# Kernel tuning notes

Hardware: AMD Instinct MI355X
Metric: run time of the kernel (lower is better)

Reference implementation:

```python
import jax, jax.numpy as jnp
import numpy as np

N, D, E, K, L, NF, VOCAB = 100000, 128, 600000, 3, 3, 9, 100
BN_EPS = 1e-5
S = 0.05


def setup_inputs() -> dict:
    key = jax.random.key(0)
    ks = jax.random.split(key, 8)
    return {
        "x": jax.random.randint(ks[0], (N, NF), 0, VOCAB),
        "k_edges": jax.random.randint(ks[1], (K, 2, E), 0, N),
        "emb_tables": jax.random.normal(ks[2], (NF, VOCAB, D), jnp.float32) * S,
        "W1": jax.random.normal(ks[3], (L, D, 2 * D), jnp.float32) * S,
        "b1": jnp.zeros((L, 2 * D), jnp.float32),
        "g1": jnp.ones((L, 2 * D), jnp.float32),
        "be1": jnp.zeros((L, 2 * D), jnp.float32),
        "W2": jax.random.normal(ks[4], (L, 2 * D, D), jnp.float32) * S,
        "b2": jnp.zeros((L, D), jnp.float32),
        "eps": jnp.zeros((L,), jnp.float32),
        "alpha": jnp.zeros((L, K), jnp.float32),
        "bn_g": jnp.ones((L, D), jnp.float32),
        "bn_b": jnp.zeros((L, D), jnp.float32),
    }


def _bn(h, g, b):
    # training-mode BatchNorm1d over the node (batch) axis
    mu = h.mean(axis=0)
    var = h.var(axis=0)
    return (h - mu) * jax.lax.rsqrt(var + BN_EPS) * g + b


def _gin(h, src, dst, eps_l, W1_l, b1_l, g1_l, be1_l, W2_l, b2_l):
    # NodeGINConv (train_eps): mlp((1+eps)*x + sum_{j->i} x_j)
    agg = jax.ops.segment_sum(h[src], dst, num_segments=N)  # [N, D]
    z = (1.0 + eps_l) * h + agg
    z = jax.nn.relu(_bn(z @ W1_l + b1_l, g1_l, be1_l))  # [N, 2D]
    return z @ W2_l + b2_l  # [N, D]


def reference(x, k_edges, emb_tables, W1, b1, g1, be1, W2, b2, eps, alpha, bn_g, bn_b):
    # AtomEncoder: sum of per-feature embedding lookups -> [N, D]
    h = jnp.take_along_axis(
        emb_tables.transpose(1, 0, 2),  # [VOCAB, NF, D]
        x.T[..., None].transpose(1, 0, 2) * 0 + 0,  # placeholder avoided below
        axis=0,
    ) if False else emb_tables[jnp.arange(NF)[None, :], x].sum(axis=1)
    for l in range(L):
        # one shared wrapped GIN conv applied to each of the K relational edge sets
        msgs = jax.vmap(
            lambda e: _gin(h, e[0], e[1], eps[l], W1[l], b1[l], g1[l], be1[l], W2[l], b2[l])
        )(k_edges)  # [K, N, D]
        a = jax.nn.softmax(alpha[l])  # [K]
        h = jnp.einsum('knd,k->nd', msgs, a)
        h = jax.nn.relu(_bn(h, bn_g[l], bn_b[l]))  # dropout p=0 / eval -> identity
    return h
```

## Files before the change

### kernel.cpp

```cpp
#include <hip/hip_runtime.h>

#define NV     100000
#define DD     128
#define D2     256
#define EE     600000
#define KK     3
#define LL     3
#define NFEAT  9
#define VOCABS 100

#define NBKT   196
#define BCAP   8192

typedef __attribute__((ext_vector_type(8))) short short8;
typedef __attribute__((ext_vector_type(4))) float f32x4;
typedef __attribute__((ext_vector_type(2))) float f32x2;
typedef __attribute__((ext_vector_type(4))) unsigned int uint4v;

#define PA      0
#define PA2     8
#define PB2     136
#define PA1K(k) (264 + (k)*512)
#define PB1K(k) (264 + (k)*512 + 256)

#define ZS(k)  ((k)*512)
#define ZQ(k)  ((k)*512 + 256)
#define HSUM   1536
#define HSQ    1664

#define HB_OFF   ((size_t)0)
#define ZIN_OFF  ((size_t)25700000)
#define HNB_OFF  ((size_t)102500000)
#define O_BASE   ((size_t)128100000)

__device__ __forceinline__ unsigned short f2bf(float f) {
    union { float f; unsigned int u; } v; v.f = f;
    return (unsigned short)((v.u + 0x7FFFu + ((v.u >> 16) & 1u)) >> 16);
}
__device__ __forceinline__ float bf2f(unsigned short u) {
    union { unsigned int u; float f; } v; v.u = ((unsigned int)u) << 16;
    return v.f;
}
__device__ __forceinline__ f32x2 up2(unsigned int v) {
    union { unsigned int u[2]; f32x2 f; } w;
    w.u[0] = v << 16;
    w.u[1] = v & 0xFFFF0000u;
    return w.f;
}

__global__ void k_embed(const int* __restrict__ x, const float* __restrict__ emb,
                        unsigned short* __restrict__ hb) {
    int id = blockIdx.x*256 + threadIdx.x;
    int n = id >> 5, q = id & 31;
    if (n >= NV) {
        if (n < NV + 8) *(unsigned long long*)(hb + (size_t)n*DD + q*4) = 0ull;
        return;
    }
    const int* xr = x + n*NFEAT;
    f32x4 acc = {0.f,0.f,0.f,0.f};
    #pragma unroll
    for (int f = 0; f < NFEAT; ++f) {
        int idx = xr[f];
        acc += *(const f32x4*)(emb + ((size_t)(f*VOCABS + idx)*DD + q*4));
    }
    unsigned short pk[4];
    pk[0] = f2bf(acc[0]); pk[1] = f2bf(acc[1]); pk[2] = f2bf(acc[2]); pk[3] = f2bf(acc[3]);
    *(unsigned long long*)(hb + (size_t)n*DD + q*4) = *(unsigned long long*)pk;
}

__global__ void kA_bin(const int* __restrict__ ke, int* __restrict__ cursor,
                       uint2* __restrict__ pairs) {
    __shared__ int hist[NBKT], excl[NBKT], ofs[NBKT], gbase[NBKT];
    __shared__ int sc[256];
    __shared__ uint2 buf[4096];
    const int rel = blockIdx.y, t = threadIdx.x;
    const int e0 = blockIdx.x * 4096;
    const int cnt = min(4096, EE - e0);
    const int* srcA = ke + (size_t)(rel*2)*EE + e0;
    const int* dstA = ke + (size_t)(rel*2+1)*EE + e0;
    if (t < NBKT) hist[t] = 0;
    __syncthreads();
    for (int i = t; i < cnt; i += 256) atomicAdd(&hist[dstA[i] >> 9], 1);
    __syncthreads();
    const int hv = (t < NBKT) ? hist[t] : 0;
    sc[t] = hv;
    for (int off = 1; off < 256; off <<= 1) {
        __syncthreads();
        int v = (t >= off) ? sc[t-off] : 0;
        __syncthreads();
        sc[t] += v;
    }
    __syncthreads();
    if (t < NBKT) {
        excl[t] = sc[t] - hv;
        ofs[t]  = sc[t] - hv;
        if (hv > 0) gbase[t] = atomicAdd(&cursor[rel*NBKT + t], hv);
    }
    __syncthreads();
    for (int i = t; i < cnt; i += 256) {
        unsigned int s = (unsigned int)srcA[i], d = (unsigned int)dstA[i];
        int p = atomicAdd(&ofs[d >> 9], 1);
        uint2 u; u.x = s; u.y = d;
        buf[p] = u;
    }
    __syncthreads();
    for (int i = t; i < cnt; i += 256) {
        uint2 u = buf[i];
        int b = (int)(u.y >> 9);
        int pos = gbase[b] + (i - excl[b]);
        if (pos < BCAP) pairs[(size_t)(rel*NBKT + b)*BCAP + pos] = u;
    }
}

__global__ void kB_scan(const int* __restrict__ cursor, int* __restrict__ ebase) {
    __shared__ int sc[256];
    const int t = threadIdx.x;
    for (int rel = 0; rel < KK; ++rel) {
        int hv = (t < NBKT) ? min(cursor[rel*NBKT + t], BCAP) : 0;
        sc[t] = hv;
        for (int off = 1; off < 256; off <<= 1) {
            __syncthreads();
            int v = (t >= off) ? sc[t-off] : 0;
            __syncthreads();
            sc[t] += v;
        }
        __syncthreads();
        if (t < NBKT) ebase[rel*NBKT + t] = sc[t] - hv;
        __syncthreads();
    }
}

__global__ void kB_fill(const uint2* __restrict__ pairs, const int* __restrict__ cursor,
                        const int* __restrict__ ebase, int* __restrict__ rp,
                        int* __restrict__ col) {
    __shared__ int h2[512], excl[512], cur[512], sc[256];
    const int b = blockIdx.x, rel = blockIdx.y, t = threadIdx.x;
    const int lo = b * 512;
    const int cnt = min(cursor[rel*NBKT + b], BCAP);
    const int base = ebase[rel*NBKT + b];
    const uint2* P = pairs + (size_t)(rel*NBKT + b)*BCAP;
    h2[t] = 0; h2[t+256] = 0; cur[t] = 0; cur[t+256] = 0;
    __syncthreads();
    for (int i = t; i < cnt; i += 256) atomicAdd(&h2[(int)P[i].y - lo], 1);
    __syncthreads();
    const int a0 = h2[2*t], a1 = h2[2*t+1];
    sc[t] = a0 + a1;
    for (int off = 1; off < 256; off <<= 1) {
        __syncthreads();
        int v = (t >= off) ? sc[t-off] : 0;
        __syncthreads();
        sc[t] += v;
    }
    __syncthreads();
    const int e2 = sc[t] - (a0 + a1);
    excl[2*t] = e2; excl[2*t+1] = e2 + a0;
    __syncthreads();
    for (int tt = t; tt < 512; tt += 256) {
        int n = lo + tt;
        if (n <= NV) rp[(size_t)rel*(NV+1) + n] = base + excl[tt];
    }
    for (int i = t; i < cnt; i += 256) {
        uint2 u = P[i];
        int r = (int)u.y - lo;
        int p = atomicAdd(&cur[r], 1);
        col[(size_t)rel*EE + base + excl[r] + p] = (int)u.x;
    }
}

__global__ void k_prep(const float* __restrict__ W1, const float* __restrict__ W2,
                       const float* __restrict__ alpha, const int l,
                       unsigned short* __restrict__ w1f, unsigned short* __restrict__ w2f,
                       float* __restrict__ params) {
    int id = blockIdx.x*256 + threadIdx.x;
    if (id == 0) {
        float a0 = alpha[l*KK+0], a1 = alpha[l*KK+1], a2 = alpha[l*KK+2];
        float m = fmaxf(a0, fmaxf(a1, a2));
        float e0 = expf(a0-m), e1 = expf(a1-m), e2 = expf(a2-m);
        float inv = 1.f/(e0+e1+e2);
        params[PA+0] = e0*inv; params[PA+1] = e1*inv; params[PA+2] = e2*inv;
    }
    if (id < 4096) {
        int kt = id >> 10, nt = (id >> 6) & 15, lane = id & 63;
        int r = lane & 15, g = lane >> 4;
        const float* Wl = W1 + (size_t)l*DD*D2;
        #pragma unroll
        for (int e = 0; e < 8; ++e) {
            int kk = kt*32 + g*8 + e, c = nt*16 + r;
            w1f[(size_t)id*8 + e] = f2bf(Wl[(size_t)kk*D2 + c]);
        }
    } else if (id < 8192) {
        int id2 = id - 4096;
        int kt = id2 >> 9, nt = (id2 >> 6) & 7, lane = id2 & 63;
        int r = lane & 15, g = lane >> 4;
        const float* Wl = W2 + (size_t)l*D2*DD;
        #pragma unroll
        for (int e = 0; e < 8; ++e) {
            int kk = kt*32 + g*8 + e, c = nt*16 + r;
            w2f[(size_t)id2*8 + e] = f2bf(Wl[(size_t)kk*DD + c]);
        }
    }
}

__global__ void k_gather3(const unsigned short* __restrict__ hb, const int* __restrict__ rp,
                          const int* __restrict__ col, const float* __restrict__ epsp,
                          unsigned short* __restrict__ zin) {
    int gid = blockIdx.x*256 + threadIdx.x;
    int n0 = gid >> 6;
    if (n0 >= NV) return;
    const int n = __builtin_amdgcn_readfirstlane(n0);
    const int lane = threadIdx.x & 63;
    const int q = lane >> 4, r = lane & 15;
    const int r16 = r << 4;
    const char* hbase = (const char*)hb;
    const float epsv = 1.0f + epsp[0];
    const uint4v sv = *(const uint4v*)(hbase + (((unsigned)n << 8) + r16));
    int b0[KK], dg[KK], cv[KK];
    #pragma unroll
    for (int k = 0; k < KK; ++k) {
        int a = rp[k*(NV+1) + n];
        int b = rp[k*(NV+1) + n + 1];
        b0[k] = a; dg[k] = b - a;
        cv[k] = (lane < dg[k]) ? col[(size_t)k*EE + a + lane] : NV;
    }
    f32x2 acc[KK][4];
    #pragma unroll
    for (int k = 0; k < KK; ++k)
        #pragma unroll
        for (int c = 0; c < 4; ++c) acc[k][c] = (f32x2){0.f, 0.f};
    #pragma unroll
    for (int k = 0; k < KK; ++k) {
        const int dc = min(dg[k], 64);
        for (int base = 0; base < dc; base += 8) {
            int s0 = __shfl(cv[k], base + q);
            int s1 = __shfl(cv[k], base + q + 4);
            uint4v v0 = *(const uint4v*)(hbase + (((unsigned)s0 << 8) + r16));
            uint4v v1 = *(const uint4v*)(hbase + (((unsigned)s1 << 8) + r16));
            #pragma unroll
            for (int c = 0; c < 4; ++c) {
                acc[k][c] += up2(v0[c]);
                acc[k][c] += up2(v1[c]);
            }
        }
        for (int j = b0[k] + 64 + q; j < b0[k] + dg[k]; j += 4) {
            int s0 = col[(size_t)k*EE + j];
            uint4v v0 = *(const uint4v*)(hbase + (((unsigned)s0 << 8) + r16));
            #pragma unroll
            for (int c = 0; c < 4; ++c) acc[k][c] += up2(v0[c]);
        }
    }
    #pragma unroll
    for (int k = 0; k < KK; ++k) {
        #pragma unroll
        for (int c = 0; c < 4; ++c) {
            acc[k][c][0] += __shfl_xor(acc[k][c][0], 16);
            acc[k][c][1] += __shfl_xor(acc[k][c][1], 16);
            acc[k][c][0] += __shfl_xor(acc[k][c][0], 32);
            acc[k][c][1] += __shfl_xor(acc[k][c][1], 32);
        }
    }
    if (q == 0) {
        #pragma unroll
        for (int k = 0; k < KK; ++k) {
            uint4v pk;
            #pragma unroll
            for (int c = 0; c < 4; ++c) {
                f32x2 s2 = up2(sv[c]);
                float lo = acc[k][c][0] + epsv * s2[0];
                float hi = acc[k][c][1] + epsv * s2[1];
                unsigned int pko;
                asm("v_cvt_pk_bf16_f32 %0, %1, %2" : "=v"(pko) : "v"(lo), "v"(hi));
                pk[c] = pko;
            }
            *(uint4v*)((char*)zin + (size_t)k*NV*DD*2 + (((unsigned)n << 8) + r16)) = pk;
        }
    }
}

__launch_bounds__(256, 2)
__global__ void k_stats3(const unsigned short* __restrict__ zin,
                         const unsigned short* __restrict__ w1f,
                         float* __restrict__ stats) {
    __shared__ __align__(16) unsigned short bfr1[32768];
    __shared__ float scf[1024];
    const int t = threadIdx.x;
    const int krel = blockIdx.y;
    const unsigned short* zk = zin + (size_t)krel*NV*DD;
    float* zsum = stats + ZS(krel);
    float* zsq  = stats + ZQ(krel);
    for (int i = t; i < 4096; i += 256)
        *(uint4v*)(bfr1 + i*8) = *(const uint4v*)(w1f + i*8);
    const int lane = t & 63, w = t >> 6;
    const int r_ = lane & 15, g = lane >> 4;
    const int rt = w & 1, ch = w >> 1;
    __syncthreads();
    float ssum[8] = {0,0,0,0,0,0,0,0};
    float ssq[8]  = {0,0,0,0,0,0,0,0};
    for (int tile = blockIdx.x; tile < NV/32; tile += gridDim.x) {
        const int row0 = tile*32;
        short8 af[4];
        #pragma unroll
        for (int kt = 0; kt < 4; ++kt)
            af[kt] = *(const short8*)(zk + (size_t)(row0 + rt*16 + r_)*DD + kt*32 + g*8);
        #pragma unroll
        for (int ct = 0; ct < 8; ++ct) {
            const int ntg = ch*8 + ct;
            f32x4 c = {0.f,0.f,0.f,0.f};
            #pragma unroll
            for (int kt = 0; kt < 4; ++kt) {
                short8 b = *(const short8*)(bfr1 + ((size_t)((kt*16 + ntg)*64 + lane))*8);
                c = __builtin_amdgcn_mfma_f32_16x16x32_bf16(af[kt], b, c, 0, 0, 0);
            }
            float s = c[0]+c[1]+c[2]+c[3];
            float q = c[0]*c[0]+c[1]*c[1]+c[2]*c[2]+c[3]*c[3];
            s += __shfl_xor(s, 16); q += __shfl_xor(q, 16);
            s += __shfl_xor(s, 32); q += __shfl_xor(q, 32);
            ssum[ct] += s; ssq[ct] += q;
        }
    }
    if (g == 0) {
        #pragma unroll
        for (int ct = 0; ct < 8; ++ct) {
            const int colc = (ch*8 + ct)*16 + r_;
            scf[rt*256 + colc]       = ssum[ct];
            scf[512 + rt*256 + colc] = ssq[ct];
        }
    }
    __syncthreads();
    atomicAdd(zsum + t, scf[t]       + scf[256 + t]);
    atomicAdd(zsq  + t, scf[512 + t] + scf[768 + t]);
}

__global__ void k_bnprep3(float* __restrict__ stats,
                          const float* __restrict__ g1l, const float* __restrict__ be1l,
                          float* __restrict__ params) {
    int j = threadIdx.x;
    #pragma unroll
    for (int k = 0; k < KK; ++k) {
        float ak  = params[PA + k];
        float mu  = stats[ZS(k) + j] * (1.0f/NV);
        float var = stats[ZQ(k) + j] * (1.0f/NV) - mu*mu;
        float A = g1l[j] * rsqrtf(var + 1e-5f);
        params[PA1K(k) + j] = ak * A;
        params[PB1K(k) + j] = ak * (be1l[j] - mu*A);
        stats[ZS(k) + j] = 0.0f; stats[ZQ(k) + j] = 0.0f;
    }
}

#define LOAD_AF(AF, TILE) {                                                        \
    const int rowp_ = (TILE)*32;                                                   \
    _Pragma("unroll")                                                              \
    for (int k = 0; k < KK; ++k) {                                                 \
        _Pragma("unroll")                                                          \
        for (int kt = 0; kt < 4; ++kt)                                             \
            AF[k][kt] = *(const short8*)(zin + (size_t)k*NV*DD                     \
                          + (size_t)(rowp_ + rt*16 + r_)*DD + kt*32 + g*8);        \
    }                                                                              \
}

#define GBODY(AF, AFN, YT) {                                                       \
    const int cur_ = tile, nx_ = tile + step;                                      \
    f32x4 y[4];                                                                    \
    _Pragma("unroll")                                                              \
    for (int ct = 0; ct < 4; ++ct) y[ct] = (f32x4){0.f,0.f,0.f,0.f};               \
    _Pragma("unroll")                                                              \
    for (int k = 0; k < KK; ++k) {                                                 \
        _Pragma("unroll")                                                          \
        for (int ct = 0; ct < 4; ++ct) {                                           \
            const int ntg = ch*4 + ct;                                             \
            f32x4 c = {0.f,0.f,0.f,0.f};                                           \
            _Pragma("unroll")                                                      \
            for (int kt = 0; kt < 4; ++kt) {                                       \
                short8 b = *(const short8*)(bfr1 + ((size_t)((kt*16 + ntg)*64 + lane))*8); \
                c = __builtin_amdgcn_mfma_f32_16x16x32_bf16(AF[k][kt], b, c, 0, 0, 0); \
            }                                                                      \
            _Pragma("unroll")                                                      \
            for (int reg = 0; reg < 4; ++reg)                                      \
                y[ct][reg] += fmaxf(pa1[k][ct]*c[reg] + pb1[k][ct], 0.0f);         \
        }                                                                          \
    }                                                                              \
    if (nx_ < NT) LOAD_AF(AFN, nx_);                                               \
    _Pragma("unroll")                                                              \
    for (int ct = 0; ct < 4; ++ct) {                                               \
        const int col2 = ((ch*4 + ct)*16 + r_)*2;                                  \
        _Pragma("unroll")                                                          \
        for (int reg = 0; reg < 4; ++reg) {                                        \
            const int row = rt*16 + g*4 + reg;                                     \
            *(unsigned short*)(YT + row*512 + (col2 ^ ((row & 15) << 4))) = f2bf(y[ct][reg]); \
        }                                                                          \
    }                                                                              \
    __syncthreads();                                                               \
    short8 ya[8];                                                                  \
    _Pragma("unroll")                                                              \
    for (int kt = 0; kt < 8; ++kt)                                                 \
        ya[kt] = *(const short8*)(YT + arow*512 + ((kt*64 + g*16) ^ ((arow & 15) << 4))); \
    _Pragma("unroll")                                                              \
    for (int ct2 = 0; ct2 < 2; ++ct2) {                                            \
        const int ntg2 = ch*2 + ct2;                                               \
        f32x4 c = {0.f,0.f,0.f,0.f};                                               \
        _Pragma("unroll")                                                          \
        for (int kt = 0; kt < 8; ++kt) {                                           \
            short8 b = *(const short8*)(bfr2 + ((size_t)((kt*8 + ntg2)*64 + lane))*8); \
            c = __builtin_amdgcn_mfma_f32_16x16x32_bf16(ya[kt], b, c, 0, 0, 0);    \
        }                                                                          \
        unsigned short* hp = hnb + (size_t)(cur_*32 + rt*16 + g*4)*DD + ntg2*16 + r_; \
        float ps = 0.0f, pq = 0.0f;                                                \
        _Pragma("unroll")                                                          \
        for (int reg = 0; reg < 4; ++reg) {                                        \
            float xv = c[reg];                                                     \
            hp[(size_t)reg*DD] = f2bf(xv);                                         \
            ps += xv; pq += xv*xv;                                                 \
        }                                                                          \
        ps += __shfl_xor(ps, 16); pq += __shfl_xor(pq, 16);                        \
        ps += __shfl_xor(ps, 32); pq += __shfl_xor(pq, 32);                        \
        ssum[ct2] += ps; ssq[ct2] += pq;                                           \
    }                                                                              \
    tile = nx_;                                                                    \
}

__launch_bounds__(512, 1)
__global__ void k_gemm2f(const unsigned short* __restrict__ zin,
                         const unsigned short* __restrict__ w1f,
                         const unsigned short* __restrict__ w2f,
                         const float* __restrict__ params,
                         unsigned short* __restrict__ hnb,
                         float* __restrict__ hsum, float* __restrict__ hsq) {
    __shared__ __align__(16) unsigned short bfr1[32768];
    __shared__ __align__(16) unsigned short bfr2[32768];
    __shared__ __align__(16) unsigned char ytA[16384];
    __shared__ __align__(16) unsigned char ytB[16384];
    const int t = threadIdx.x;
    for (int i = t; i < 4096; i += 512)
        *(uint4v*)(bfr1 + i*8) = *(const uint4v*)(w1f + i*8);
    for (int i = t; i < 4096; i += 512)
        *(uint4v*)(bfr2 + i*8) = *(const uint4v*)(w2f + i*8);
    const int lane = t & 63, w = t >> 6;
    const int r_ = lane & 15, g = lane >> 4;
    const int rt = w & 1, ch = w >> 1;
    const int arow = rt*16 + r_;
    float pa1[KK][4], pb1[KK][4];
    #pragma unroll
    for (int k = 0; k < KK; ++k) {
        #pragma unroll
        for (int ct = 0; ct < 4; ++ct) {
            const int colc = (ch*4 + ct)*16 + r_;
            pa1[k][ct] = params[PA1K(k) + colc];
            pb1[k][ct] = params[PB1K(k) + colc];
        }
    }
    __syncthreads();
    float ssum[2] = {0,0}, ssq[2] = {0,0};
    const int NT = NV/32;
    const int step = gridDim.x;
    int tile = blockIdx.x;
    short8 afA[KK][4], afB[KK][4];
    LOAD_AF(afA, tile);
    while (tile < NT) {
        GBODY(afA, afB, ytA);
        if (tile >= NT) break;
        GBODY(afB, afA, ytB);
    }
    __syncthreads();
    float* scf = (float*)ytA;
    if (g == 0) {
        #pragma unroll
        for (int ct2 = 0; ct2 < 2; ++ct2) {
            scf[w*32 + ct2*16 + r_]       = ssum[ct2];
            scf[256 + w*32 + ct2*16 + r_] = ssq[ct2];
        }
    }
    __syncthreads();
    if (t < 128) {
        const int chc = t >> 5, idx = t & 31;
        float s = 0.0f, q = 0.0f;
        #pragma unroll
        for (int rr = 0; rr < 2; ++rr) {
            s += scf[(chc*2 + rr)*32 + idx];
            q += scf[256 + (chc*2 + rr)*32 + idx];
        }
        atomicAdd(hsum + t, s);
        atomicAdd(hsq + t, q);
    }
}

__global__ void k_bnprep2(float* __restrict__ hsum, float* __restrict__ hsq,
                          const float* __restrict__ bng, const float* __restrict__ bnb,
                          float* __restrict__ params) {
    int j = threadIdx.x;
    float mu  = hsum[j] * (1.0f/NV);
    float var = hsq[j]  * (1.0f/NV) - mu*mu;
    float A = bng[j] * rsqrtf(var + 1e-5f);
    params[PA2 + j] = A;
    params[PB2 + j] = bnb[j] - mu*A;
    hsum[j] = 0.0f; hsq[j] = 0.0f;
}

__global__ void k_bnapply_mid(const unsigned short* __restrict__ hnb,
                              const float* __restrict__ params,
                              unsigned short* __restrict__ hb) {
    int id = blockIdx.x*256 + threadIdx.x;
    const int col0 = (id & 15)*8;
    short8 v = *(const short8*)(hnb + (size_t)id*8);
    f32x4 A0 = *(const f32x4*)(params + PA2 + col0);
    f32x4 A1 = *(const f32x4*)(params + PA2 + col0 + 4);
    f32x4 B0 = *(const f32x4*)(params + PB2 + col0);
    f32x4 B1 = *(const f32x4*)(params + PB2 + col0 + 4);
    short8 o;
    #pragma unroll
    for (int j = 0; j < 4; ++j) {
        o[j]   = (short)f2bf(fmaxf(A0[j]*bf2f((unsigned short)v[j])   + B0[j], 0.0f));
        o[j+4] = (short)f2bf(fmaxf(A1[j]*bf2f((unsigned short)v[j+4]) + B1[j], 0.0f));
    }
    *(short8*)(hb + (size_t)id*8) = o;
}

__global__ void k_bnapply_fin(const unsigned short* __restrict__ hnb,
                              const float* __restrict__ params,
                              float* __restrict__ out) {
    int id = blockIdx.x*256 + threadIdx.x;
    const int col0 = (id & 15)*8;
    short8 v = *(const short8*)(hnb + (size_t)id*8);
    f32x4 A0 = *(const f32x4*)(params + PA2 + col0);
    f32x4 A1 = *(const f32x4*)(params + PA2 + col0 + 4);
    f32x4 B0 = *(const f32x4*)(params + PB2 + col0);
    f32x4 B1 = *(const f32x4*)(params + PB2 + col0 + 4);
    f32x4 o0, o1;
    #pragma unroll
    for (int j = 0; j < 4; ++j) {
        o0[j] = fmaxf(A0[j]*bf2f((unsigned short)v[j])   + B0[j], 0.0f);
        o1[j] = fmaxf(A1[j]*bf2f((unsigned short)v[j+4]) + B1[j], 0.0f);
    }
    *(f32x4*)(out + (size_t)id*8)     = o0;
    *(f32x4*)(out + (size_t)id*8 + 4) = o1;
}

extern "C" void kernel_launch(void* const* d_in, const int* in_sizes, int n_in,
                              void* d_out, int out_size, void* d_ws, size_t ws_size,
                              hipStream_t stream) {
    const int*   x     = (const int*)d_in[0];
    const int*   ke    = (const int*)d_in[1];
    const float* emb   = (const float*)d_in[2];
    const float* W1    = (const float*)d_in[3];
    const float* g1    = (const float*)d_in[5];
    const float* be1   = (const float*)d_in[6];
    const float* W2    = (const float*)d_in[7];
    const float* eps   = (const float*)d_in[9];
    const float* alpha = (const float*)d_in[10];
    const float* bng   = (const float*)d_in[11];
    const float* bnb   = (const float*)d_in[12];

    char* ws = (char*)d_ws;
    unsigned short* hb     = (unsigned short*)(ws + HB_OFF);
    unsigned short* zin    = (unsigned short*)(ws + ZIN_OFF);
    unsigned short* hnb    = (unsigned short*)(ws + HNB_OFF);
    size_t o = O_BASE;
    unsigned short* w1f    = (unsigned short*)(ws + o);          o += 65536;
    unsigned short* w2f    = (unsigned short*)(ws + o);          o += 65536;
    float*          stats  = (float*)(ws + o);                   o += 8192;
    float*          params = (float*)(ws + o);                   o += 8192;
    int*            rp     = (int*)(ws + o);                     o += 1200128;
    int*            col    = (int*)(ws + o);                     o += 7200000;
    int*            cur    = (int*)(ws + o);                     o += 4096;
    int*            ebase  = (int*)(ws + o);                     o += 4096;
    uint2*          pairs  = (uint2*)(ws + ZIN_OFF);

    k_embed<<<12501, 256, 0, stream>>>(x, emb, hb);

    hipMemsetAsync(cur, 0, KK*NBKT*sizeof(int), stream);
    hipMemsetAsync(stats, 0, 8192, stream);
    kA_bin<<<dim3(147, KK), 256, 0, stream>>>(ke, cur, pairs);
    kB_scan<<<1, 256, 0, stream>>>(cur, ebase);
    kB_fill<<<dim3(NBKT, KK), 256, 0, stream>>>(pairs, cur, ebase, rp, col);

    for (int l = 0; l < LL; ++l) {
        k_prep<<<32, 256, 0, stream>>>(W1, W2, alpha, l, w1f, w2f, params);
        k_gather3<<<25000, 256, 0, stream>>>(hb, rp, col, eps + l, zin);
        k_stats3<<<dim3(512, KK), 256, 0, stream>>>(zin, w1f, stats);
        k_bnprep3<<<1, 256, 0, stream>>>(stats, g1 + l*D2, be1 + l*D2, params);
        k_gemm2f<<<256, 512, 0, stream>>>(zin, w1f, w2f, params, hnb,
                                          stats + HSUM, stats + HSQ);
        k_bnprep2<<<1, 128, 0, stream>>>(stats + HSUM, stats + HSQ,
                                         bng + l*DD, bnb + l*DD, params);
        if (l < LL-1) k_bnapply_mid<<<6250, 256, 0, stream>>>(hnb, params, hb);
        else          k_bnapply_fin<<<6250, 256, 0, stream>>>(hnb, params, (float*)d_out);
    }
}
```

Measured before the change: 786.6 us.

## Double k_gemm2f block to 1024 threads and drop register prefetch of A tiles

```diff
diff --git a/kernel.cpp b/kernel.cpp
--- a/kernel.cpp
+++ b/kernel.cpp
@@ -346,42 +346,38 @@
     }
 }
 
-#define LOAD_AF(AF, TILE) {                                                        \
-    const int rowp_ = (TILE)*32;                                                   \
+#define GBODY2(YT) {                                                               \
+    const int cur_ = tile;                                                         \
+    short8 af[KK][4];                                                              \
     _Pragma("unroll")                                                              \
     for (int k = 0; k < KK; ++k) {                                                 \
         _Pragma("unroll")                                                          \
         for (int kt = 0; kt < 4; ++kt)                                             \
-            AF[k][kt] = *(const short8*)(zin + (size_t)k*NV*DD                     \
-                          + (size_t)(rowp_ + rt*16 + r_)*DD + kt*32 + g*8);        \
+            af[k][kt] = *(const short8*)(zin + (size_t)k*NV*DD                     \
+                          + (size_t)(cur_*32 + rt*16 + r_)*DD + kt*32 + g*8);      \
     }                                                                              \
-}
-
-#define GBODY(AF, AFN, YT) {                                                       \
-    const int cur_ = tile, nx_ = tile + step;                                      \
-    f32x4 y[4];                                                                    \
-    _Pragma("unroll")                                                              \
-    for (int ct = 0; ct < 4; ++ct) y[ct] = (f32x4){0.f,0.f,0.f,0.f};               \
+    f32x4 y[2];                                                                    \
+    y[0] = (f32x4){0.f,0.f,0.f,0.f};                                               \
+    y[1] = (f32x4){0.f,0.f,0.f,0.f};                                               \
     _Pragma("unroll")                                                              \
     for (int k = 0; k < KK; ++k) {                                                 \
         _Pragma("unroll")                                                          \
-        for (int ct = 0; ct < 4; ++ct) {                                           \
-            const int ntg = ch*4 + ct;                                             \
+        for (int ct = 0; ct < 2; ++ct) {                                           \
+            const int ntg = ch*2 + ct;                                             \
             f32x4 c = {0.f,0.f,0.f,0.f};                                           \
             _Pragma("unroll")                                                      \
             for (int kt = 0; kt < 4; ++kt) {                                       \
                 short8 b = *(const short8*)(bfr1 + ((size_t)((kt*16 + ntg)*64 + lane))*8); \
-                c = __builtin_amdgcn_mfma_f32_16x16x32_bf16(AF[k][kt], b, c, 0, 0, 0); \
+                c = __builtin_amdgcn_mfma_f32_16x16x32_bf16(af[k][kt], b, c, 0, 0, 0); \
             }                                                                      \
             _Pragma("unroll")                                                      \
             for (int reg = 0; reg < 4; ++reg)                                      \
                 y[ct][reg] += fmaxf(pa1[k][ct]*c[reg] + pb1[k][ct], 0.0f);         \
         }                                                                          \
     }                                                                              \
-    if (nx_ < NT) LOAD_AF(AFN, nx_);                                               \
     _Pragma("unroll")                                                              \
-    for (int ct = 0; ct < 4; ++ct) {                                               \
-        const int col2 = ((ch*4 + ct)*16 + r_)*2;                                  \
+    for (int ct = 0; ct < 2; ++ct) {                                               \
+        const int col2 = ((ch*2 + ct)*16 + r_)*2;                                  \
         _Pragma("unroll")                                                          \
         for (int reg = 0; reg < 4; ++reg) {                                        \
             const int row = rt*16 + g*4 + reg;                                     \
@@ -393,31 +389,27 @@
     _Pragma("unroll")                                                              \
     for (int kt = 0; kt < 8; ++kt)                                                 \
         ya[kt] = *(const short8*)(YT + arow*512 + ((kt*64 + g*16) ^ ((arow & 15) << 4))); \
+    f32x4 c2 = {0.f,0.f,0.f,0.f};                                                  \
     _Pragma("unroll")                                                              \
-    for (int ct2 = 0; ct2 < 2; ++ct2) {                                            \
-        const int ntg2 = ch*2 + ct2;                                               \
-        f32x4 c = {0.f,0.f,0.f,0.f};                                               \
-        _Pragma("unroll")                                                          \
-        for (int kt = 0; kt < 8; ++kt) {                                           \
-            short8 b = *(const short8*)(bfr2 + ((size_t)((kt*8 + ntg2)*64 + lane))*8); \
-            c = __builtin_amdgcn_mfma_f32_16x16x32_bf16(ya[kt], b, c, 0, 0, 0);    \
-        }                                                                          \
-        unsigned short* hp = hnb + (size_t)(cur_*32 + rt*16 + g*4)*DD + ntg2*16 + r_; \
-        float ps = 0.0f, pq = 0.0f;                                                \
-        _Pragma("unroll")                                                          \
-        for (int reg = 0; reg < 4; ++reg) {                                        \
-            float xv = c[reg];                                                     \
-            hp[(size_t)reg*DD] = f2bf(xv);                                         \
-            ps += xv; pq += xv*xv;                                                 \
-        }                                                                          \
-        ps += __shfl_xor(ps, 16); pq += __shfl_xor(pq, 16);                        \
-        ps += __shfl_xor(ps, 32); pq += __shfl_xor(pq, 32);                        \
-        ssum[ct2] += ps; ssq[ct2] += pq;                                           \
+    for (int kt = 0; kt < 8; ++kt) {                                               \
+        short8 b = *(const short8*)(bfr2 + ((size_t)((kt*8 + ch)*64 + lane))*8);   \
+        c2 = __builtin_amdgcn_mfma_f32_16x16x32_bf16(ya[kt], b, c2, 0, 0, 0);      \
     }                                                                              \
-    tile = nx_;                                                                    \
-}
-
-__launch_bounds__(512, 1)
+    unsigned short* hp = hnb + (size_t)(cur_*32 + rt*16 + g*4)*DD + ch*16 + r_;    \
+    float ps = 0.0f, pq = 0.0f;                                                    \
+    _Pragma("unroll")                                                              \
+    for (int reg = 0; reg < 4; ++reg) {                                            \
+        float xv = c2[reg];                                                        \
+        hp[(size_t)reg*DD] = f2bf(xv);                                             \
+        ps += xv; pq += xv*xv;                                                     \
+    }                                                                              \
+    ps += __shfl_xor(ps, 16); pq += __shfl_xor(pq, 16);                            \
+    ps += __shfl_xor(ps, 32); pq += __shfl_xor(pq, 32);                            \
+    ssum0 += ps; ssq0 += pq;                                                       \
+    tile += step;                                                                  \
+}
+
+__launch_bounds__(1024, 1)
 __global__ void k_gemm2f(const unsigned short* __restrict__ zin,
                          const unsigned short* __restrict__ w1f,
                          const unsigned short* __restrict__ w2f,
@@ -429,56 +421,44 @@
     __shared__ __align__(16) unsigned char ytA[16384];
     __shared__ __align__(16) unsigned char ytB[16384];
     const int t = threadIdx.x;
-    for (int i = t; i < 4096; i += 512)
+    for (int i = t; i < 4096; i += 1024)
         *(uint4v*)(bfr1 + i*8) = *(const uint4v*)(w1f + i*8);
-    for (int i = t; i < 4096; i += 512)
+    for (int i = t; i < 4096; i += 1024)
         *(uint4v*)(bfr2 + i*8) = *(const uint4v*)(w2f + i*8);
     const int lane = t & 63, w = t >> 6;
     const int r_ = lane & 15, g = lane >> 4;
     const int rt = w & 1, ch = w >> 1;
     const int arow = rt*16 + r_;
-    float pa1[KK][4], pb1[KK][4];
+    float pa1[KK][2], pb1[KK][2];
     #pragma unroll
     for (int k = 0; k < KK; ++k) {
         #pragma unroll
-        for (int ct = 0; ct < 4; ++ct) {
-            const int colc = (ch*4 + ct)*16 + r_;
+        for (int ct = 0; ct < 2; ++ct) {
+            const int colc = (ch*2 + ct)*16 + r_;
             pa1[k][ct] = params[PA1K(k) + colc];
             pb1[k][ct] = params[PB1K(k) + colc];
         }
     }
     __syncthreads();
-    float ssum[2] = {0,0}, ssq[2] = {0,0};
+    float ssum0 = 0.0f, ssq0 = 0.0f;
     const int NT = NV/32;
     const int step = gridDim.x;
     int tile = blockIdx.x;
-    short8 afA[KK][4], afB[KK][4];
-    LOAD_AF(afA, tile);
     while (tile < NT) {
-        GBODY(afA, afB, ytA);
+        GBODY2(ytA);
         if (tile >= NT) break;
-        GBODY(afB, afA, ytB);
+        GBODY2(ytB);
     }
     __syncthreads();
     float* scf = (float*)ytA;
     if (g == 0) {
-        #pragma unroll
-        for (int ct2 = 0; ct2 < 2; ++ct2) {
-            scf[w*32 + ct2*16 + r_]       = ssum[ct2];
-            scf[256 + w*32 + ct2*16 + r_] = ssq[ct2];
-        }
+        scf[rt*128 + ch*16 + r_]       = ssum0;
+        scf[256 + rt*128 + ch*16 + r_] = ssq0;
     }
     __syncthreads();
     if (t < 128) {
-        const int chc = t >> 5, idx = t & 31;
-        float s = 0.0f, q = 0.0f;
-        #pragma unroll
-        for (int rr = 0; rr < 2; ++rr) {
-            s += scf[(chc*2 + rr)*32 + idx];
-            q += scf[256 + (chc*2 + rr)*32 + idx];
-        }
-        atomicAdd(hsum + t, s);
-        atomicAdd(hsq + t, q);
+        atomicAdd(hsum + t, scf[t]       + scf[128 + t]);
+        atomicAdd(hsq  + t, scf[256 + t] + scf[384 + t]);
     }
 }
 
@@ -576,8 +556,8 @@
         k_gather3<<<25000, 256, 0, stream>>>(hb, rp, col, eps + l, zin);
         k_stats3<<<dim3(512, KK), 256, 0, stream>>>(zin, w1f, stats);
         k_bnprep3<<<1, 256, 0, stream>>>(stats, g1 + l*D2, be1 + l*D2, params);
-        k_gemm2f<<<256, 512, 0, stream>>>(zin, w1f, w2f, params, hnb,
-                                          stats + HSUM, stats + HSQ);
+        k_gemm2f<<<256, 1024, 0, stream>>>(zin, w1f, w2f, params, hnb,
+                                           stats + HSUM, stats + HSQ);
         k_bnprep2<<<1, 128, 0, stream>>>(stats + HSUM, stats + HSQ,
                                          bng + l*DD, bnb + l*DD, params);
         if (l < LL-1) k_bnapply_mid<<<6250, 256, 0, stream>>>(hnb, params, hb);
```

Measured after the change: 803.0 us. 2.1% more time.
